# Performance work log

Hardware: AMD Instinct MI355X
Metric: run time of the kernel (lower is better)

## Reference

```python
import jax, jax.numpy as jnp
import numpy as np

B, N, D, H, DM = 4, 1024, 1024, 16, 4096
DH = D // H
SCALE = DH ** -0.5
EPS = 1e-5


def layer_norm(x, g, b):
    mu = jnp.mean(x, axis=-1, keepdims=True)
    var = jnp.mean((x - mu) ** 2, axis=-1, keepdims=True)
    return (x - mu) * jax.lax.rsqrt(var + EPS) * g + b


def mha(q_in, k_in, v_in, Wq, bq, Wk, bk, Wv, bv, Wp, bp):
    # weights stored (in, out); torch Linear equivalent y = x @ W + b
    q = (q_in @ Wq + bq).reshape(B, -1, H, DH).transpose(0, 2, 1, 3)  # (B,H,Nq,DH)
    k = (k_in @ Wk + bk).reshape(B, -1, H, DH).transpose(0, 2, 1, 3)
    v = (v_in @ Wv + bv).reshape(B, -1, H, DH).transpose(0, 2, 1, 3)
    attn = jax.nn.softmax(jnp.einsum('bhqd,bhkd->bhqk', q, k) * SCALE, axis=-1)
    x = jnp.einsum('bhqk,bhkd->bhqd', attn, v).transpose(0, 2, 1, 3).reshape(B, -1, D)
    return x @ Wp + bp


def setup_inputs() -> dict:
    key = jax.random.key(0)
    ks = jax.random.split(key, 32)
    s = 0.02
    inp = {
        'tokens_enc': jax.random.normal(ks[0], (B, N, D), jnp.float32),
        'tokens_dec': jax.random.normal(ks[1], (B, N, D), jnp.float32),
        'PE_enc': jax.random.normal(ks[2], (B, N, D), jnp.float32),
        'PE_dec': jax.random.normal(ks[3], (B, N, D), jnp.float32),
    }
    names = ['sa_Wq', 'sa_Wk', 'sa_Wv', 'sa_Wp', 'ca_Wq', 'ca_Wk', 'ca_Wv', 'ca_Wp']
    for i, n in enumerate(names):
        inp[n] = jax.random.normal(ks[4 + i], (D, D), jnp.float32) * s
        inp[n.replace('W', 'b')] = jnp.zeros((D,), jnp.float32)
    inp['mlp_W1'] = jax.random.normal(ks[12], (D, DM), jnp.float32) * s
    inp['mlp_b1'] = jnp.zeros((DM,), jnp.float32)
    inp['mlp_W2'] = jax.random.normal(ks[13], (DM, D), jnp.float32) * s
    inp['mlp_b2'] = jnp.zeros((D,), jnp.float32)
    for i in (1, 2, 3):
        inp[f'ln{i}_g'] = jnp.ones((D,), jnp.float32)
        inp[f'ln{i}_b'] = jnp.zeros((D,), jnp.float32)
    return inp


def reference(tokens_enc, tokens_dec, PE_enc, PE_dec,
              sa_Wq, sa_bq, sa_Wk, sa_bk, sa_Wv, sa_bv, sa_Wp, sa_bp,
              ca_Wq, ca_bq, ca_Wk, ca_bk, ca_Wv, ca_bv, ca_Wp, ca_bp,
              mlp_W1, mlp_b1, mlp_W2, mlp_b2,
              ln1_g, ln1_b, ln2_g, ln2_b, ln3_g, ln3_b):
    # SA (pre-norm): q=k=ln(x)+PE_dec, v=ln(x)
    x2 = layer_norm(tokens_dec, ln1_g, ln1_b)
    qk = x2 + PE_dec
    tokens_dec = tokens_dec + mha(qk, qk, x2, sa_Wq, sa_bq, sa_Wk, sa_bk, sa_Wv, sa_bv, sa_Wp, sa_bp)
    # CA: q=ln(x)+PE_dec, k=enc+PE_enc, v=enc
    x2 = layer_norm(tokens_dec, ln2_g, ln2_b)
    tokens_dec = tokens_dec + mha(x2 + PE_dec, tokens_enc + PE_enc, tokens_enc,
                                  ca_Wq, ca_bq, ca_Wk, ca_bk, ca_Wv, ca_bv, ca_Wp, ca_bp)
    # FFD
    x2 = layer_norm(tokens_dec, ln3_g, ln3_b)
    h = jax.nn.gelu(x2 @ mlp_W1 + mlp_b1, approximate=False)
    return tokens_dec + (h @ mlp_W2 + mlp_b2)
```

## Files before the change

### kernel.cpp

```cpp
#include <hip/hip_runtime.h>
#include <hip/hip_bf16.h>
#include <math.h>

#define B_ 4
#define N_ 1024
#define D_ 1024
#define H_ 16
#define DH_ 64
#define DM_ 4096
#define NT_ (B_*N_)
#define EPS_ 1e-5f
#define SCALE_ 0.125f
#define CEXP_ 0.1803368801111244f

typedef unsigned short u16;
typedef short s16x8 __attribute__((ext_vector_type(8)));
typedef __bf16 y16x8 __attribute__((ext_vector_type(8)));
typedef float f32x4 __attribute__((ext_vector_type(4)));
typedef float f32x16 __attribute__((ext_vector_type(16)));

#define ZERO16 (f32x16){0.f,0.f,0.f,0.f,0.f,0.f,0.f,0.f,0.f,0.f,0.f,0.f,0.f,0.f,0.f,0.f}

__device__ __forceinline__ u16 f2bs(float f) {
  unsigned int u = __builtin_bit_cast(unsigned int, f);
  u += 0x7fffu + ((u >> 16) & 1u);
  return (u16)(u >> 16);
}

static __device__ __forceinline__ f32x4 MFMA(y16x8 a, y16x8 b, f32x4 c) {
  return __builtin_amdgcn_mfma_f32_16x16x32_bf16(a, b, c, 0, 0, 0);
}
static __device__ __forceinline__ f32x16 MFMA32(y16x8 a, y16x8 b, f32x16 c) {
  return __builtin_amdgcn_mfma_f32_32x32x16_bf16(a, b, c, 0, 0, 0);
}

static __device__ __forceinline__ unsigned cvtpk(float a, float b) {
  unsigned r;
  asm("v_cvt_pk_bf16_f32 %0, %1, %2" : "=v"(r) : "v"(a), "v"(b));
  return r;
}

static __device__ __forceinline__ void async16(void* lds, const void* g) {
  __builtin_amdgcn_global_load_lds(
      (const __attribute__((address_space(1))) unsigned int*)g,
      (__attribute__((address_space(3))) unsigned int*)lds, 16, 0, 0);
}

__global__ __launch_bounds__(256) void k_prep(
    const float* __restrict__ s0, const float* __restrict__ s1,
    const float* __restrict__ s2, const float* __restrict__ s3,
    const float* __restrict__ s4, const float* __restrict__ s5,
    const float* __restrict__ s6, const float* __restrict__ s7,
    u16* __restrict__ w8, const float* __restrict__ mW1,
    u16* __restrict__ w1T, const float* __restrict__ mW2,
    u16* __restrict__ w2T, const float* __restrict__ enc,
    const float* __restrict__ pe, u16* __restrict__ encpe,
    u16* __restrict__ encv,
    const float* __restrict__ xdec, const float* __restrict__ g1,
    const float* __restrict__ bta1, const float* __restrict__ pedec,
    u16* __restrict__ x2o, u16* __restrict__ qko) {
  __shared__ __align__(16) u16 tile[128][72];
  __shared__ float red[8];
  const int gid = blockIdx.x;
  const int t = threadIdx.x;
  if (gid < 2048) {
    const float* W;
    u16* Wt;
    int K, Ncols, k0, n0;
    if (gid < 1024) {
      int z = gid >> 7, rem = gid & 127;
      W = z == 0 ? s0 : z == 1 ? s1 : z == 2 ? s2 : z == 3 ? s3
        : z == 4 ? s4 : z == 5 ? s5 : z == 6 ? s6 : s7;
      Wt = w8 + (size_t)z * D_ * D_;
      K = D_; Ncols = D_;
      k0 = (rem & 15) * 64; n0 = (rem >> 4) * 128;
    } else if (gid < 1536) {
      int rem = gid - 1024;
      W = mW1; Wt = w1T; K = D_; Ncols = DM_;
      k0 = (rem & 15) * 64; n0 = (rem >> 4) * 128;
    } else {
      int rem = gid - 1536;
      W = mW2; Wt = w2T; K = DM_; Ncols = D_;
      k0 = (rem & 63) * 64; n0 = (rem >> 6) * 128;
    }
    const int l32 = t & 31, rk = t >> 5;
#pragma unroll
    for (int i = 0; i < 8; ++i) {
      int k = i * 8 + rk;
      float4 v = *(const float4*)(W + (size_t)(k0 + k) * Ncols + n0 + l32 * 4);
      tile[l32 * 4 + 0][k] = f2bs(v.x);
      tile[l32 * 4 + 1][k] = f2bs(v.y);
      tile[l32 * 4 + 2][k] = f2bs(v.z);
      tile[l32 * 4 + 3][k] = f2bs(v.w);
    }
    __syncthreads();
    const int nr = t >> 3, c = t & 7;
#pragma unroll
    for (int p = 0; p < 4; ++p) {
      int n = p * 32 + nr;
      *(s16x8*)(Wt + (size_t)(n0 + n) * K + k0 + c * 8) =
          *(const s16x8*)&tile[n][c * 8];
    }
  } else if (gid < 6144) {
    int i = (gid - 2048) * 256 + t;
    float4 e = ((const float4*)enc)[i];
    float4 p = ((const float4*)pe)[i];
    union { u16 u[4]; uint2 v; } a, b;
    a.u[0] = f2bs(e.x + p.x); a.u[1] = f2bs(e.y + p.y);
    a.u[2] = f2bs(e.z + p.z); a.u[3] = f2bs(e.w + p.w);
    b.u[0] = f2bs(e.x); b.u[1] = f2bs(e.y); b.u[2] = f2bs(e.z); b.u[3] = f2bs(e.w);
    ((uint2*)encpe)[i] = a.v;
    ((uint2*)encv)[i] = b.v;
  } else {
    int row = gid - 6144;
    float4 v = ((const float4*)(xdec + (size_t)row * D_))[t];
    float s = v.x + v.y + v.z + v.w;
#pragma unroll
    for (int o = 1; o < 64; o <<= 1) s += __shfl_xor(s, o, 64);
    if ((t & 63) == 0) red[t >> 6] = s;
    __syncthreads();
    float mean = (red[0] + red[1] + red[2] + red[3]) * (1.0f / D_);
    float dx = v.x - mean, dy = v.y - mean, dz = v.z - mean, dw = v.w - mean;
    float s2 = dx * dx + dy * dy + dz * dz + dw * dw;
#pragma unroll
    for (int o = 1; o < 64; o <<= 1) s2 += __shfl_xor(s2, o, 64);
    if ((t & 63) == 0) red[4 + (t >> 6)] = s2;
    __syncthreads();
    float var = (red[4] + red[5] + red[6] + red[7]) * (1.0f / D_);
    float rstd = rsqrtf(var + EPS_);
    float4 gv = ((const float4*)g1)[t];
    float4 bv = ((const float4*)bta1)[t];
    float y0 = dx * rstd * gv.x + bv.x;
    float y1 = dy * rstd * gv.y + bv.y;
    float y2 = dz * rstd * gv.z + bv.z;
    float y3 = dw * rstd * gv.w + bv.w;
    union { u16 u[4]; uint2 v2; } o1;
    o1.u[0] = f2bs(y0); o1.u[1] = f2bs(y1); o1.u[2] = f2bs(y2); o1.u[3] = f2bs(y3);
    ((uint2*)(x2o + (size_t)row * D_))[t] = o1.v2;
    float4 pv = ((const float4*)(pedec + (size_t)row * D_))[t];
    union { u16 u[4]; uint2 v2; } o2;
    o2.u[0] = f2bs(y0 + pv.x); o2.u[1] = f2bs(y1 + pv.y);
    o2.u[2] = f2bs(y2 + pv.z); o2.u[3] = f2bs(y3 + pv.w);
    ((uint2*)(qko + (size_t)row * D_))[t] = o2.v2;
  }
}

__global__ __launch_bounds__(256) void k_ln(const float* __restrict__ x,
                                            const float* __restrict__ g,
                                            const float* __restrict__ bta,
                                            const float* __restrict__ pe,
                                            u16* __restrict__ x2o,
                                            u16* __restrict__ qko) {
  int row = blockIdx.x;
  int t = threadIdx.x;
  float4 v = ((const float4*)(x + (size_t)row * D_))[t];
  float s = v.x + v.y + v.z + v.w;
#pragma unroll
  for (int o = 1; o < 64; o <<= 1) s += __shfl_xor(s, o, 64);
  __shared__ float red[8];
  if ((t & 63) == 0) red[t >> 6] = s;
  __syncthreads();
  float mean = (red[0] + red[1] + red[2] + red[3]) * (1.0f / D_);
  float dx = v.x - mean, dy = v.y - mean, dz = v.z - mean, dw = v.w - mean;
  float s2 = dx * dx + dy * dy + dz * dz + dw * dw;
#pragma unroll
  for (int o = 1; o < 64; o <<= 1) s2 += __shfl_xor(s2, o, 64);
  if ((t & 63) == 0) red[4 + (t >> 6)] = s2;
  __syncthreads();
  float var = (red[4] + red[5] + red[6] + red[7]) * (1.0f / D_);
  float rstd = rsqrtf(var + EPS_);
  float4 gv = ((const float4*)g)[t];
  float4 bv = ((const float4*)bta)[t];
  float y0 = dx * rstd * gv.x + bv.x;
  float y1 = dy * rstd * gv.y + bv.y;
  float y2 = dz * rstd * gv.z + bv.z;
  float y3 = dw * rstd * gv.w + bv.w;
  union { u16 u[4]; uint2 v2; } o1;
  o1.u[0] = f2bs(y0); o1.u[1] = f2bs(y1); o1.u[2] = f2bs(y2); o1.u[3] = f2bs(y3);
  ((uint2*)(x2o + (size_t)row * D_))[t] = o1.v2;
  if (pe) {
    float4 pv = ((const float4*)(pe + (size_t)row * D_))[t];
    union { u16 u[4]; uint2 v2; } o2;
    o2.u[0] = f2bs(y0 + pv.x); o2.u[1] = f2bs(y1 + pv.y);
    o2.u[2] = f2bs(y2 + pv.z); o2.u[3] = f2bs(y3 + pv.w);
    ((uint2*)(qko + (size_t)row * D_))[t] = o2.v2;
  }
}

template <int EPI, int BM>
__global__ __launch_bounds__(512) void k_gemm(const u16* __restrict__ A,
                                              const u16* __restrict__ Bt,
                                              const float* __restrict__ bias,
                                              const float* __restrict__ res,
                                              float* __restrict__ outf,
                                              u16* __restrict__ outb,
                                              int M, int Nn, int K, int ldo) {
  constexpr int BN = 128, BK = 64;
  constexpr int FM = BM / 32;
  __shared__ __align__(128) char smem[2][(BM + BN) * BK * 2];
  const int t = threadIdx.x;
  const int wave = t >> 6, lane = t & 63, lg = lane >> 4, lc = lane & 15;
  const int nwg = gridDim.x * gridDim.y;
  const int bid = blockIdx.y * gridDim.x + blockIdx.x;
  const int lb = (bid & 7) * (nwg >> 3) + (bid >> 3);
  const int bx = lb % gridDim.x, by = lb / gridDim.x;
  const int m0 = by * BM, n0 = bx * BN;
  const int wm = (wave >> 2) * (BM / 2), wn = (wave & 3) * 32;
  f32x4 acc[FM][2];
#pragma unroll
  for (int i = 0; i < FM; ++i)
#pragma unroll
    for (int j = 0; j < 2; ++j) acc[i][j] = (f32x4){0.f, 0.f, 0.f, 0.f};
  const char* Ag = (const char*)(A + (size_t)m0 * K);
  const char* Bg = (const char*)(Bt + (size_t)n0 * K);
  const int sr = t >> 3, sp = t & 7;

  auto stage = [&](int bufi, int kt) {
    char* sA = smem[bufi];
    char* sB = smem[bufi] + BM * BK * 2;
#pragma unroll
    for (int rr = 0; rr < BM / 64; ++rr) {
      int row = rr * 64 + sr;
      int c = sp ^ (row & 7);
      async16(sA + (size_t)row * 128 + sp * 16,
              Ag + ((size_t)row * K + kt + c * 8) * 2);
    }
#pragma unroll
    for (int rr = 0; rr < 2; ++rr) {
      int row = rr * 64 + sr;
      int c = sp ^ (row & 7);
      async16(sB + (size_t)row * 128 + sp * 16,
              Bg + ((size_t)row * K + kt + c * 8) * 2);
    }
  };
  auto compute = [&](int bufi) {
    const char* sA = smem[bufi];
    const char* sB = smem[bufi] + BM * BK * 2;
#pragma unroll
    for (int ks = 0; ks < 2; ++ks) {
      y16x8 af[FM], bfr[2];
#pragma unroll
      for (int fm = 0; fm < FM; ++fm) {
        int R = wm + fm * 16 + lc;
        int pc = (ks * 4 + lg) ^ (R & 7);
        af[fm] = *(const y16x8*)(sA + (size_t)R * 128 + pc * 16);
      }
#pragma unroll
      for (int fn = 0; fn < 2; ++fn) {
        int R = wn + fn * 16 + lc;
        int pc = (ks * 4 + lg) ^ (R & 7);
        bfr[fn] = *(const y16x8*)(sB + (size_t)R * 128 + pc * 16);
      }
#pragma unroll
      for (int fm = 0; fm < FM; ++fm)
#pragma unroll
        for (int fn = 0; fn < 2; ++fn)
          acc[fm][fn] = MFMA(af[fm], bfr[fn], acc[fm][fn]);
    }
  };

  stage(0, 0);
  __syncthreads();
  int cur = 0;
  for (int kt = BK; kt < K; kt += BK) {
    stage(cur ^ 1, kt);
    compute(cur);
    __syncthreads();
    cur ^= 1;
  }
  compute(cur);

#pragma unroll
  for (int fm = 0; fm < FM; ++fm)
#pragma unroll
    for (int fn = 0; fn < 2; ++fn)
#pragma unroll
      for (int j = 0; j < 4; ++j) {
        int row = m0 + wm + fm * 16 + lg * 4 + j;
        int col = n0 + wn + fn * 16 + lc;
        float vv = acc[fm][fn][j] + bias[col];
        size_t idx = (size_t)row * ldo + col;
        if constexpr (EPI == 0) {
          outb[idx] = f2bs(vv);
        } else if constexpr (EPI == 1) {
          outf[idx] = vv + res[idx];
        } else {
          float gx = 0.5f * vv * (1.0f + erff(vv * 0.70710678118f));
          outb[idx] = f2bs(gx);
        }
      }
}

__global__ __launch_bounds__(512) void k_gemmG(
    const u16* __restrict__ A0, const u16* __restrict__ A1,
    const u16* __restrict__ A2, const u16* __restrict__ A3,
    const u16* __restrict__ A4, const u16* __restrict__ W0,
    const u16* __restrict__ W1, const u16* __restrict__ W2,
    const u16* __restrict__ W3, const u16* __restrict__ W4,
    const float* __restrict__ b0, const float* __restrict__ b1,
    const float* __restrict__ b2, const float* __restrict__ b3,
    const float* __restrict__ b4, u16* __restrict__ qk1,
    u16* __restrict__ vt1, u16* __restrict__ qk2, u16* __restrict__ vt2) {
  constexpr int BM = 128, BN = 128, BK = 64, K = D_;
  __shared__ __align__(128) char smem[2][(BM + BN) * BK * 2];
  const int z = blockIdx.z;
  const u16* A = z == 0 ? A0 : z == 1 ? A1 : z == 2 ? A2 : z == 3 ? A3 : A4;
  const u16* Bt = z == 0 ? W0 : z == 1 ? W1 : z == 2 ? W2 : z == 3 ? W3 : W4;
  const float* bias = z == 0 ? b0 : z == 1 ? b1 : z == 2 ? b2 : z == 3 ? b3 : b4;
  const int t = threadIdx.x;
  const int wave = t >> 6, lane = t & 63, lg = lane >> 4, lc = lane & 15;
  const int nwg = gridDim.x * gridDim.y;
  const int bid = blockIdx.y * gridDim.x + blockIdx.x;
  const int lb = (bid & 7) * (nwg >> 3) + (bid >> 3);
  const int bx = lb % gridDim.x, by = lb / gridDim.x;
  const int m0 = by * BM, n0 = bx * BN;
  const int wm = (wave >> 2) * 64, wn = (wave & 3) * 32;
  f32x4 acc[4][2];
#pragma unroll
  for (int i = 0; i < 4; ++i)
#pragma unroll
    for (int j = 0; j < 2; ++j) acc[i][j] = (f32x4){0.f, 0.f, 0.f, 0.f};
  const char* Ag = (const char*)(A + (size_t)m0 * K);
  const char* Bg = (const char*)(Bt + (size_t)n0 * K);
  const int sr = t >> 3, sp = t & 7;

  auto stage = [&](int bufi, int kt) {
    char* sA = smem[bufi];
    char* sB = smem[bufi] + BM * BK * 2;
#pragma unroll
    for (int rr = 0; rr < 2; ++rr) {
      int row = rr * 64 + sr;
      int c = sp ^ (row & 7);
      async16(sA + (size_t)row * 128 + sp * 16,
              Ag + ((size_t)row * K + kt + c * 8) * 2);
      async16(sB + (size_t)row * 128 + sp * 16,
              Bg + ((size_t)row * K + kt + c * 8) * 2);
    }
  };
  auto compute = [&](int bufi) {
    const char* sA = smem[bufi];
    const char* sB = smem[bufi] + BM * BK * 2;
#pragma unroll
    for (int ks = 0; ks < 2; ++ks) {
      y16x8 af[4], bfr[2];
#pragma unroll
      for (int fm = 0; fm < 4; ++fm) {
        int R = wm + fm * 16 + lc;
        int pc = (ks * 4 + lg) ^ (R & 7);
        af[fm] = *(const y16x8*)(sA + (size_t)R * 128 + pc * 16);
      }
#pragma unroll
      for (int fn = 0; fn < 2; ++fn) {
        int R = wn + fn * 16 + lc;
        int pc = (ks * 4 + lg) ^ (R & 7);
        bfr[fn] = *(const y16x8*)(sB + (size_t)R * 128 + pc * 16);
      }
#pragma unroll
      for (int fm = 0; fm < 4; ++fm)
#pragma unroll
        for (int fn = 0; fn < 2; ++fn)
          acc[fm][fn] = MFMA(af[fm], bfr[fn], acc[fm][fn]);
    }
  };

  stage(0, 0);
  __syncthreads();
  int cur = 0;
  for (int kt = BK; kt < K; kt += BK) {
    stage(cur ^ 1, kt);
    compute(cur);
    __syncthreads();
    cur ^= 1;
  }
  compute(cur);

  const bool isV = (z == 2) || (z == 4);
  if (!isV) {
    u16* outqk = (z == 3) ? qk2 : qk1;
    const int coff = (z == 1 || z == 3) ? D_ : 0;
#pragma unroll
    for (int fm = 0; fm < 4; ++fm)
#pragma unroll
      for (int fn = 0; fn < 2; ++fn)
#pragma unroll
        for (int j = 0; j < 4; ++j) {
          int row = m0 + wm + fm * 16 + lg * 4 + j;
          int col = n0 + wn + fn * 16 + lc;
          outqk[(size_t)row * (2 * D_) + coff + col] =
              f2bs(acc[fm][fn][j] + bias[col]);
        }
  } else {
    u16* outvt = (z == 2) ? vt1 : vt2;
#pragma unroll
    for (int fm = 0; fm < 4; ++fm)
#pragma unroll
      for (int fn = 0; fn < 2; ++fn) {
        int row0 = m0 + wm + fm * 16 + lg * 4;
        int col = n0 + wn + fn * 16 + lc;
        int bb = row0 >> 10, nn = row0 & (N_ - 1);
        int h = col >> 6, dh = col & 63;
        float bcol = bias[col];
        union { u16 u[4]; uint2 v; } pk;
#pragma unroll
        for (int j = 0; j < 4; ++j) pk.u[j] = f2bs(acc[fm][fn][j] + bcol);
        *(uint2*)&outvt[(((size_t)bb * H_ + h) * DH_ + dh) * N_ + nn] = pk.v;
      }
  }
}

__global__ __launch_bounds__(256) void k_attn(const u16* __restrict__ q, int qs,
                                              const u16* __restrict__ k, int ks2,
                                              const u16* __restrict__ vt,
                                              u16* __restrict__ out) {
  __shared__ __align__(16) u16 Kl[128][64];
  __shared__ __align__(16) u16 Vl[64][128];
  __shared__ __align__(16) u16 Ol[4][32][72];
  const int lb = blockIdx.x;
  const int bh = (lb & 7) | ((lb >> 6) << 3);
  const int qb = (lb >> 3) & 7;
  const int b = bh >> 4, h = bh & 15;
  const int t = threadIdx.x, wave = t >> 6, lane = t & 63;
  const int ql = lane & 31, hi = lane >> 5;
  const int q0 = qb * 128 + wave * 32;
  const u16* qp = q + ((size_t)b * N_ + q0) * qs + h * DH_;
  const u16* kp = k + (size_t)b * N_ * ks2 + h * DH_;
  const u16* vp = vt + ((size_t)bh * DH_) * N_;

  y16x8 aq[4];
#pragma unroll
  for (int s = 0; s < 4; ++s)
    aq[s] = *(const y16x8*)(qp + (size_t)ql * qs + s * 16 + hi * 8);

  f32x16 o0 = ZERO16, o1 = ZERO16;
  float m_r = -1e30f, l_r = 0.f;

  const int kr = t >> 3, kc = t & 7;
  const int vr = t >> 4, vc = t & 15;
  s16x8 kreg[4], vreg[4];
#pragma unroll
  for (int rr = 0; rr < 4; ++rr) {
    kreg[rr] = *(const s16x8*)(kp + (size_t)(rr * 32 + kr) * ks2 + kc * 8);
    vreg[rr] = *(const s16x8*)(vp + (size_t)(rr * 16 + vr) * N_ + vc * 8);
  }

  for (int kt = 0; kt < N_; kt += 128) {
    __syncthreads();
#pragma unroll
    for (int rr = 0; rr < 4; ++rr) {
      int krow = rr * 32 + kr;
      *(s16x8*)&Kl[krow][(kc ^ (krow & 7)) * 8] = kreg[rr];
      int vrow = rr * 16 + vr;
      *(s16x8*)&Vl[vrow][(vc ^ (vrow & 15)) * 8] = vreg[rr];
    }
    __syncthreads();
    if (kt + 128 < N_) {
#pragma unroll
      for (int rr = 0; rr < 4; ++rr) {
        kreg[rr] = *(const s16x8*)(kp + (size_t)(kt + 128 + rr * 32 + kr) * ks2 + kc * 8);
        vreg[rr] = *(const s16x8*)(vp + (size_t)(rr * 16 + vr) * N_ + kt + 128 + vc * 8);
      }
    }

#pragma unroll
    for (int sub = 0; sub < 2; ++sub) {
      f32x16 st0 = ZERO16, st1 = ZERO16;
      __builtin_amdgcn_s_setprio(1);
#pragma unroll
      for (int s = 0; s < 4; ++s) {
        int pc0 = ((s * 2 + hi) ^ (ql & 7)) * 8;
        y16x8 ak0 = *(const y16x8*)&Kl[sub * 64 + ql][pc0];
        y16x8 ak1 = *(const y16x8*)&Kl[sub * 64 + 32 + ql][pc0];
        st0 = MFMA32(ak0, aq[s], st0);
        st1 = MFMA32(ak1, aq[s], st1);
      }
      __builtin_amdgcn_s_setprio(0);

      float mx = st0[0];
#pragma unroll
      for (int r = 1; r < 16; ++r) mx = fmaxf(mx, st0[r]);
#pragma unroll
      for (int r = 0; r < 16; ++r) mx = fmaxf(mx, st1[r]);
      mx = fmaxf(mx, __shfl_xor(mx, 32, 64));
      if (!__all(mx - m_r <= 32.f)) {
        float mn = fmaxf(m_r, mx);
        float corr = exp2f((m_r - mn) * CEXP_);
        l_r *= corr;
        o0 = o0 * corr;
        o1 = o1 * corr;
        m_r = mn;
      }
      float ps = 0.f;
#pragma unroll
      for (int r = 0; r < 16; ++r) {
        float e = exp2f((st0[r] - m_r) * CEXP_); st0[r] = e; ps += e;
      }
#pragma unroll
      for (int r = 0; r < 16; ++r) {
        float e = exp2f((st1[r] - m_r) * CEXP_); st1[r] = e; ps += e;
      }
      ps += __shfl_xor(ps, 32, 64);
      l_r += ps;

      __builtin_amdgcn_s_setprio(1);
#pragma unroll
      for (int ks = 0; ks < 4; ++ks) {
        unsigned A0, A1, B0, B1;
        if (ks < 2) {
          const int il = ks * 8;
          A0 = cvtpk(st0[il + 0], st0[il + 1]);
          A1 = cvtpk(st0[il + 2], st0[il + 3]);
          B0 = cvtpk(st0[il + 4], st0[il + 5]);
          B1 = cvtpk(st0[il + 6], st0[il + 7]);
        } else {
          const int il = (ks - 2) * 8;
          A0 = cvtpk(st1[il + 0], st1[il + 1]);
          A1 = cvtpk(st1[il + 2], st1[il + 3]);
          B0 = cvtpk(st1[il + 4], st1[il + 5]);
          B1 = cvtpk(st1[il + 6], st1[il + 7]);
        }
        asm("v_permlane32_swap_b32 %0, %1" : "+v"(A0), "+v"(B0));
        asm("v_permlane32_swap_b32 %0, %1" : "+v"(A1), "+v"(B1));
        union { unsigned w[4]; y16x8 v; } fr;
        fr.w[0] = A0; fr.w[1] = A1; fr.w[2] = B0; fr.w[3] = B1;
        int ch0 = (sub * 8 + ks * 2 + hi) ^ (ql & 15);
        int ch1 = (sub * 8 + ks * 2 + hi) ^ ((32 + ql) & 15);
        y16x8 bv0 = *(const y16x8*)&Vl[ql][ch0 * 8];
        y16x8 bv1 = *(const y16x8*)&Vl[32 + ql][ch1 * 8];
        o0 = MFMA32(bv0, fr.v, o0);
        o1 = MFMA32(bv1, fr.v, o1);
      }
      __builtin_amdgcn_s_setprio(0);
    }
  }

  float rl = 1.f / l_r;
#pragma unroll
  for (int rq = 0; rq < 4; ++rq)
#pragma unroll
    for (int e = 0; e < 4; e += 2) {
      *(unsigned*)&Ol[wave][ql][8 * rq + 4 * hi + e] =
          cvtpk(o0[rq * 4 + e] * rl, o0[rq * 4 + e + 1] * rl);
      *(unsigned*)&Ol[wave][ql][32 + 8 * rq + 4 * hi + e] =
          cvtpk(o1[rq * 4 + e] * rl, o1[rq * 4 + e + 1] * rl);
    }
#pragma unroll
  for (int pp = 0; pp < 4; ++pp) {
    int row = pp * 8 + (lane >> 3);
    s16x8 vv = *(const s16x8*)&Ol[wave][row][(lane & 7) * 8];
    *(s16x8*)(out + ((size_t)b * N_ + q0 + row) * D_ + h * DH_ + (lane & 7) * 8) = vv;
  }
}

extern "C" void kernel_launch(void* const* d_in, const int* in_sizes, int n_in,
                              void* d_out, int out_size, void* d_ws, size_t ws_size,
                              hipStream_t stream) {
  const float* tokens_enc = (const float*)d_in[0];
  const float* tokens_dec = (const float*)d_in[1];
  const float* PE_enc = (const float*)d_in[2];
  const float* PE_dec = (const float*)d_in[3];
  const float* sa_Wq = (const float*)d_in[4];  const float* sa_bq = (const float*)d_in[5];
  const float* sa_Wk = (const float*)d_in[6];  const float* sa_bk = (const float*)d_in[7];
  const float* sa_Wv = (const float*)d_in[8];  const float* sa_bv = (const float*)d_in[9];
  const float* sa_Wp = (const float*)d_in[10]; const float* sa_bp = (const float*)d_in[11];
  const float* ca_Wq = (const float*)d_in[12]; const float* ca_bq = (const float*)d_in[13];
  const float* ca_Wk = (const float*)d_in[14]; const float* ca_bk = (const float*)d_in[15];
  const float* ca_Wv = (const float*)d_in[16]; const float* ca_bv = (const float*)d_in[17];
  const float* ca_Wp = (const float*)d_in[18]; const float* ca_bp = (const float*)d_in[19];
  const float* mlp_W1 = (const float*)d_in[20]; const float* mlp_b1 = (const float*)d_in[21];
  const float* mlp_W2 = (const float*)d_in[22]; const float* mlp_b2 = (const float*)d_in[23];
  const float* ln1_g = (const float*)d_in[24]; const float* ln1_b = (const float*)d_in[25];
  const float* ln2_g = (const float*)d_in[26]; const float* ln2_b = (const float*)d_in[27];
  const float* ln3_g = (const float*)d_in[28]; const float* ln3_b = (const float*)d_in[29];

  char* wsp = (char*)d_ws;
  size_t off = 0;
  auto alloc = [&](size_t bytes) -> char* {
    char* p = wsp + off;
    off += (bytes + 255) & ~(size_t)255;
    return p;
  };
  u16* w8   = (u16*)alloc((size_t)8 * D_ * D_ * 2);
  u16* w1T  = (u16*)alloc((size_t)DM_ * D_ * 2);
  u16* w2T  = (u16*)alloc((size_t)D_ * DM_ * 2);
  u16* encpe = (u16*)alloc((size_t)NT_ * D_ * 2);
  u16* encv  = (u16*)alloc((size_t)NT_ * D_ * 2);
  u16* x2b = (u16*)alloc((size_t)NT_ * D_ * 2);
  u16* qkb = (u16*)alloc((size_t)NT_ * D_ * 2);
  u16* qkm = (u16*)alloc((size_t)NT_ * 2 * D_ * 2);
  u16* qkm2 = (u16*)alloc((size_t)NT_ * 2 * D_ * 2);
  u16* vtb = (u16*)alloc((size_t)NT_ * D_ * 2);
  u16* vtb2 = (u16*)alloc((size_t)NT_ * D_ * 2);
  u16* attb = (u16*)alloc((size_t)NT_ * D_ * 2);
  float* dec1 = (float*)alloc((size_t)NT_ * D_ * 4);
  float* dec2 = (float*)alloc((size_t)NT_ * D_ * 4);
  u16* hb = (u16*)alloc((size_t)NT_ * DM_ * 2);

  const size_t DD = (size_t)D_ * D_;
  u16* wqT  = w8;
  u16* wkT  = w8 + 1 * DD;
  u16* wvT  = w8 + 2 * DD;
  u16* wpT  = w8 + 3 * DD;
  u16* cwqT = w8 + 4 * DD;
  u16* cwkT = w8 + 5 * DD;
  u16* cwvT = w8 + 6 * DD;
  u16* cwpT = w8 + 7 * DD;

  k_prep<<<dim3(10240), 256, 0, stream>>>(sa_Wq, sa_Wk, sa_Wv, sa_Wp,
                                          ca_Wq, ca_Wk, ca_Wv, ca_Wp, w8,
                                          mlp_W1, w1T, mlp_W2, w2T,
                                          tokens_enc, PE_enc, encpe, encv,
                                          tokens_dec, ln1_g, ln1_b, PE_dec,
                                          x2b, qkb);

  k_gemmG<<<dim3(8, 32, 5), 512, 0, stream>>>(
      qkb, qkb, x2b, encpe, encv, wqT, wkT, wvT, cwkT, cwvT,
      sa_bq, sa_bk, sa_bv, ca_bk, ca_bv, qkm, vtb, qkm2, vtb2);
  k_attn<<<dim3(512), 256, 0, stream>>>(qkm, 2 * D_, qkm + D_, 2 * D_, vtb, attb);
  k_gemm<1, 64><<<dim3(8, 64), 512, 0, stream>>>(attb, wpT, sa_bp, tokens_dec,
                                                 dec1, nullptr, NT_, D_, D_, D_);

  k_ln<<<dim3(NT_), 256, 0, stream>>>(dec1, ln2_g, ln2_b, PE_dec, x2b, qkb);
  k_gemm<0, 64><<<dim3(8, 64), 512, 0, stream>>>(qkb, cwqT, ca_bq, nullptr,
                                                 nullptr, qkm2, NT_, D_, D_, 2 * D_);
  k_attn<<<dim3(512), 256, 0, stream>>>(qkm2, 2 * D_, qkm2 + D_, 2 * D_, vtb2, attb);
  k_gemm<1, 64><<<dim3(8, 64), 512, 0, stream>>>(attb, cwpT, ca_bp, dec1,
                                                 dec2, nullptr, NT_, D_, D_, D_);

  k_ln<<<dim3(NT_), 256, 0, stream>>>(dec2, ln3_g, ln3_b, nullptr, x2b, nullptr);
  k_gemm<2, 128><<<dim3(32, 32), 512, 0, stream>>>(x2b, w1T, mlp_b1, nullptr,
                                                   nullptr, hb, NT_, DM_, D_, DM_);
  k_gemm<1, 64><<<dim3(8, 64), 512, 0, stream>>>(hb, w2T, mlp_b2, dec2,
                                                 (float*)d_out, nullptr, NT_, D_, DM_, D_);
}
```

Baseline: 326.3 us.

## Move MLP weight transposes into attention kernels as extra blocks

The MLP W1 and W2 fp32-to-bf16 transpose work is moved out of the prep kernel and into the two attention launches, which now have 512 extra blocks each that do transpose tiles and then exit. The aim is to fill idle compute units during the 512-block attention grids and shorten the serial prep kernel. The risk is that the transpose blocks compete with attention blocks for bandwidth and slots, and they reuse the attention LDS allocation.

```diff
diff --git a/kernel.cpp b/kernel.cpp
--- a/kernel.cpp
+++ b/kernel.cpp
@@ -51,9 +51,7 @@
     const float* __restrict__ s2, const float* __restrict__ s3,
     const float* __restrict__ s4, const float* __restrict__ s5,
     const float* __restrict__ s6, const float* __restrict__ s7,
-    u16* __restrict__ w8, const float* __restrict__ mW1,
-    u16* __restrict__ w1T, const float* __restrict__ mW2,
-    u16* __restrict__ w2T, const float* __restrict__ enc,
+    u16* __restrict__ w8, const float* __restrict__ enc,
     const float* __restrict__ pe, u16* __restrict__ encpe,
     u16* __restrict__ encv,
     const float* __restrict__ xdec, const float* __restrict__ g1,
@@ -63,31 +61,17 @@
   __shared__ float red[8];
   const int gid = blockIdx.x;
   const int t = threadIdx.x;
-  if (gid < 2048) {
-    const float* W;
-    u16* Wt;
-    int K, Ncols, k0, n0;
-    if (gid < 1024) {
-      int z = gid >> 7, rem = gid & 127;
-      W = z == 0 ? s0 : z == 1 ? s1 : z == 2 ? s2 : z == 3 ? s3
-        : z == 4 ? s4 : z == 5 ? s5 : z == 6 ? s6 : s7;
-      Wt = w8 + (size_t)z * D_ * D_;
-      K = D_; Ncols = D_;
-      k0 = (rem & 15) * 64; n0 = (rem >> 4) * 128;
-    } else if (gid < 1536) {
-      int rem = gid - 1024;
-      W = mW1; Wt = w1T; K = D_; Ncols = DM_;
-      k0 = (rem & 15) * 64; n0 = (rem >> 4) * 128;
-    } else {
-      int rem = gid - 1536;
-      W = mW2; Wt = w2T; K = DM_; Ncols = D_;
-      k0 = (rem & 63) * 64; n0 = (rem >> 6) * 128;
-    }
+  if (gid < 1024) {
+    int z = gid >> 7, rem = gid & 127;
+    const float* W = z == 0 ? s0 : z == 1 ? s1 : z == 2 ? s2 : z == 3 ? s3
+                   : z == 4 ? s4 : z == 5 ? s5 : z == 6 ? s6 : s7;
+    u16* Wt = w8 + (size_t)z * D_ * D_;
+    int k0 = (rem & 15) * 64, n0 = (rem >> 4) * 128;
     const int l32 = t & 31, rk = t >> 5;
 #pragma unroll
     for (int i = 0; i < 8; ++i) {
       int k = i * 8 + rk;
-      float4 v = *(const float4*)(W + (size_t)(k0 + k) * Ncols + n0 + l32 * 4);
+      float4 v = *(const float4*)(W + (size_t)(k0 + k) * D_ + n0 + l32 * 4);
       tile[l32 * 4 + 0][k] = f2bs(v.x);
       tile[l32 * 4 + 1][k] = f2bs(v.y);
       tile[l32 * 4 + 2][k] = f2bs(v.z);
@@ -98,11 +82,11 @@
 #pragma unroll
     for (int p = 0; p < 4; ++p) {
       int n = p * 32 + nr;
-      *(s16x8*)(Wt + (size_t)(n0 + n) * K + k0 + c * 8) =
+      *(s16x8*)(Wt + (size_t)(n0 + n) * D_ + k0 + c * 8) =
           *(const s16x8*)&tile[n][c * 8];
     }
-  } else if (gid < 6144) {
-    int i = (gid - 2048) * 256 + t;
+  } else if (gid < 5120) {
+    int i = (gid - 1024) * 256 + t;
     float4 e = ((const float4*)enc)[i];
     float4 p = ((const float4*)pe)[i];
     union { u16 u[4]; uint2 v; } a, b;
@@ -112,7 +96,7 @@
     ((uint2*)encpe)[i] = a.v;
     ((uint2*)encv)[i] = b.v;
   } else {
-    int row = gid - 6144;
+    int row = gid - 5120;
     float4 v = ((const float4*)(xdec + (size_t)row * D_))[t];
     float s = v.x + v.y + v.z + v.w;
 #pragma unroll
@@ -411,15 +395,44 @@
 __global__ __launch_bounds__(256) void k_attn(const u16* __restrict__ q, int qs,
                                               const u16* __restrict__ k, int ks2,
                                               const u16* __restrict__ vt,
-                                              u16* __restrict__ out) {
+                                              u16* __restrict__ out,
+                                              const float* __restrict__ Wsrc,
+                                              u16* __restrict__ Wdst,
+                                              int WK, int WNcols,
+                                              int kmask, int kshift) {
   __shared__ __align__(16) u16 Kl[128][64];
   __shared__ __align__(16) u16 Vl[64][128];
   __shared__ __align__(16) u16 Ol[4][32][72];
   const int lb = blockIdx.x;
+  const int t = threadIdx.x;
+  if (lb >= 512) {
+    u16 (*tile)[72] = reinterpret_cast<u16(*)[72]>(&Ol[0][0][0]);
+    int rem = lb - 512;
+    int k0 = (rem & kmask) * 64, n0 = (rem >> kshift) * 128;
+    const int l32 = t & 31, rk = t >> 5;
+#pragma unroll
+    for (int i = 0; i < 8; ++i) {
+      int kk = i * 8 + rk;
+      float4 v = *(const float4*)(Wsrc + (size_t)(k0 + kk) * WNcols + n0 + l32 * 4);
+      tile[l32 * 4 + 0][kk] = f2bs(v.x);
+      tile[l32 * 4 + 1][kk] = f2bs(v.y);
+      tile[l32 * 4 + 2][kk] = f2bs(v.z);
+      tile[l32 * 4 + 3][kk] = f2bs(v.w);
+    }
+    __syncthreads();
+    const int nr = t >> 3, c = t & 7;
+#pragma unroll
+    for (int p = 0; p < 4; ++p) {
+      int n = p * 32 + nr;
+      *(s16x8*)(Wdst + (size_t)(n0 + n) * WK + k0 + c * 8) =
+          *(const s16x8*)&tile[n][c * 8];
+    }
+    return;
+  }
   const int bh = (lb & 7) | ((lb >> 6) << 3);
   const int qb = (lb >> 3) & 7;
   const int b = bh >> 4, h = bh & 15;
-  const int t = threadIdx.x, wave = t >> 6, lane = t & 63;
+  const int wave = t >> 6, lane = t & 63;
   const int ql = lane & 31, hi = lane >> 5;
   const int q0 = qb * 128 + wave * 32;
   const u16* qp = q + ((size_t)b * N_ + q0) * qs + h * DH_;
@@ -605,24 +618,25 @@
   u16* cwvT = w8 + 6 * DD;
   u16* cwpT = w8 + 7 * DD;
 
-  k_prep<<<dim3(10240), 256, 0, stream>>>(sa_Wq, sa_Wk, sa_Wv, sa_Wp,
-                                          ca_Wq, ca_Wk, ca_Wv, ca_Wp, w8,
-                                          mlp_W1, w1T, mlp_W2, w2T,
-                                          tokens_enc, PE_enc, encpe, encv,
-                                          tokens_dec, ln1_g, ln1_b, PE_dec,
-                                          x2b, qkb);
+  k_prep<<<dim3(9216), 256, 0, stream>>>(sa_Wq, sa_Wk, sa_Wv, sa_Wp,
+                                         ca_Wq, ca_Wk, ca_Wv, ca_Wp, w8,
+                                         tokens_enc, PE_enc, encpe, encv,
+                                         tokens_dec, ln1_g, ln1_b, PE_dec,
+                                         x2b, qkb);
 
   k_gemmG<<<dim3(8, 32, 5), 512, 0, stream>>>(
       qkb, qkb, x2b, encpe, encv, wqT, wkT, wvT, cwkT, cwvT,
       sa_bq, sa_bk, sa_bv, ca_bk, ca_bv, qkm, vtb, qkm2, vtb2);
-  k_attn<<<dim3(512), 256, 0, stream>>>(qkm, 2 * D_, qkm + D_, 2 * D_, vtb, attb);
+  k_attn<<<dim3(1024), 256, 0, stream>>>(qkm, 2 * D_, qkm + D_, 2 * D_, vtb, attb,
+                                         mlp_W1, w1T, D_, DM_, 15, 4);
   k_gemm<1, 64><<<dim3(8, 64), 512, 0, stream>>>(attb, wpT, sa_bp, tokens_dec,
                                                  dec1, nullptr, NT_, D_, D_, D_);
 
   k_ln<<<dim3(NT_), 256, 0, stream>>>(dec1, ln2_g, ln2_b, PE_dec, x2b, qkb);
   k_gemm<0, 64><<<dim3(8, 64), 512, 0, stream>>>(qkb, cwqT, ca_bq, nullptr,
                                                  nullptr, qkm2, NT_, D_, D_, 2 * D_);
-  k_attn<<<dim3(512), 256, 0, stream>>>(qkm2, 2 * D_, qkm2 + D_, 2 * D_, vtb2, attb);
+  k_attn<<<dim3(1024), 256, 0, stream>>>(qkm2, 2 * D_, qkm2 + D_, 2 * D_, vtb2, attb,
+                                         mlp_W2, w2T, DM_, D_, 63, 6);
   k_gemm<1, 64><<<dim3(8, 64), 512, 0, stream>>>(attb, cwpT, ca_bp, dec1,
                                                  dec2, nullptr, NT_, D_, D_, D_);
 
```

After: 325.6 us. Within noise of the previous version (-0.2%).
